# Kernel optimization log

Measured on AMD Instinct MI355X. Metric: run time of the kernel, lower is better.

## Reference

```python
import jax, jax.numpy as jnp
import numpy as np

NUM_HEADS = 8
EMBED_DIM = 128
TOTAL_TOKENS = 32768  # must be divisible by NUM_HEADS; per-head seq = 4096


def setup_inputs() -> dict:
    key = jax.random.key(0)
    ks = jax.random.split(key, 7)
    E, H, T = EMBED_DIM, NUM_HEADS, TOTAL_TOKENS
    return {
        "query": jax.random.normal(ks[0], (T, E), dtype=jnp.float32),
        "key": jax.random.normal(ks[1], (T, E), dtype=jnp.float32),    # unused by the module
        "value": jax.random.normal(ks[2], (T, E), dtype=jnp.float32),  # unused by the module
        "W_qkv": jax.random.normal(ks[3], (E, 3 * E), dtype=jnp.float32) * (1.0 / np.sqrt(E)),
        "b_qkv": jax.random.normal(ks[4], (3 * E,), dtype=jnp.float32) * 0.02,
        "u_bias": jax.random.normal(ks[5], (H, E), dtype=jnp.float32) * 0.02,
        "v_bias": jax.random.normal(ks[6], (H, E), dtype=jnp.float32) * 0.02,
    }


def reference(query, key, value, W_qkv, b_qkv, u_bias, v_bias):
    H, E = NUM_HEADS, EMBED_DIM
    # Fused QKV projection (torch Linear: x @ W; W stored [in, 3*out] here)
    qkv = query @ W_qkv + b_qkv                      # [T, 3E]
    q, k, v = jnp.split(qkv, 3, axis=-1)             # each [T, E]

    def heads(x):
        # view(-1, H, E).transpose(0, 1): token axis is split across heads
        return jnp.swapaxes(x.reshape(-1, H, E), 0, 1)  # [H, S, E], S = T // H

    q = heads(q) + u_bias[:, None, :]                # per-head additive bias on q
    k = heads(k) + v_bias[:, None, :]                # per-head additive bias on k
    v = heads(v)

    scale = 1.0 / jnp.sqrt(jnp.asarray(E, dtype=q.dtype))
    scores = jnp.einsum('hse,hte->hst', q, k) * scale  # [H, S, S]
    attn = jax.nn.softmax(scores, axis=-1)
    return jnp.einsum('hst,hte->hse', attn, v)         # [H, S, E]
```

## Files before the change

### kernel.cpp

```cpp
#include <hip/hip_runtime.h>
#include <hip/hip_bf16.h>
#include <stdint.h>

#define NHEADS 8
#define SEQ    4096
#define DIM    128
#define TOK    32768

typedef __attribute__((ext_vector_type(4)))  float  f32x4;
typedef __attribute__((ext_vector_type(16))) float  f32x16;
typedef __attribute__((ext_vector_type(8)))  short  bf16x8;
typedef __attribute__((ext_vector_type(8)))  unsigned short u16x8;
typedef __attribute__((ext_vector_type(4)))  unsigned int   u32x4;

__device__ __forceinline__ unsigned short f32_to_bf16(float f) {
  union { float f; unsigned int u; } cv; cv.f = f;
  unsigned int u = cv.u;
  u += 0x7FFFu + ((u >> 16) & 1u);
  return (unsigned short)(u >> 16);
}
__device__ __forceinline__ unsigned cvtpk(float lo, float hi) {
  unsigned r;
  asm("v_cvt_pk_bf16_f32 %0, %1, %2" : "=v"(r) : "v"(lo), "v"(hi));
  return r;
}
__device__ __forceinline__ void gload16(const void* g, void* l) {
  __builtin_amdgcn_global_load_lds(
      (const __attribute__((address_space(1))) unsigned int*)g,
      (__attribute__((address_space(3))) unsigned int*)l, 16, 0, 0);
}

__global__ __launch_bounds__(256) void wt_prep_kernel(
    const float* __restrict__ W, unsigned short* __restrict__ Wt) {
  const int tid = threadIdx.x;
  const int j  = blockIdx.x * 32 + (tid >> 3);
  const int k0 = (tid & 7) * 16;
  u16x8 a, b;
  #pragma unroll
  for (int x = 0; x < 8; ++x) a[x] = f32_to_bf16(W[(size_t)(k0 + x) * 384 + j]);
  #pragma unroll
  for (int x = 0; x < 8; ++x) b[x] = f32_to_bf16(W[(size_t)(k0 + 8 + x) * 384 + j]);
  *reinterpret_cast<u16x8*>(Wt + (size_t)j * 128 + k0)     = a;
  *reinterpret_cast<u16x8*>(Wt + (size_t)j * 128 + k0 + 8) = b;
}

__global__ __launch_bounds__(256, 2) void qkv_proj_kernel(
    const float* __restrict__ qin, const unsigned short* __restrict__ Wt,
    const float* __restrict__ bqkv, const float* __restrict__ ubias,
    const float* __restrict__ vbias,
    unsigned short* __restrict__ Qh, unsigned short* __restrict__ Kh,
    unsigned short* __restrict__ Vh) {
  __shared__ __align__(16) char Xl[16384];

  const int tid  = threadIdx.x;
  const int lane = tid & 63;
  const int w    = tid >> 6;
  const int wm   = w & 1;
  const int wn   = w >> 1;
  const int col  = lane & 31;
  const int hi   = lane >> 5;
  const int tok0 = blockIdx.x * 64;

  #pragma unroll
  for (int c = 0; c < 4; ++c) {
    int idx = tid + c * 256;
    int row = idx >> 4, c16 = idx & 15;
    const float* src = qin + (size_t)(tok0 + row) * DIM + c16 * 8;
    f32x4 lo  = *reinterpret_cast<const f32x4*>(src);
    f32x4 hi4 = *reinterpret_cast<const f32x4*>(src + 4);
    u32x4 pk;
    pk[0] = cvtpk(lo[0],  lo[1]);  pk[1] = cvtpk(lo[2],  lo[3]);
    pk[2] = cvtpk(hi4[0], hi4[1]); pk[3] = cvtpk(hi4[2], hi4[3]);
    *reinterpret_cast<u32x4*>(Xl + ((row * 256 + c16 * 16) ^ ((row & 7) << 4))) = pk;
  }
  __syncthreads();

  bf16x8 af[8];
  {
    int row = wm * 32 + col;
    #pragma unroll
    for (int kk = 0; kk < 8; ++kk)
      af[kk] = *reinterpret_cast<const bf16x8*>(
          Xl + ((row * 256 + kk * 32 + hi * 16) ^ ((row & 7) << 4)));
  }

  const int s0 = blockIdx.x * 8 + wm * 4;
  const float scale = 0.1275174309f;

  #pragma unroll
  for (int nt = 0; nt < 6; ++nt) {
    const int j0 = wn * 192 + nt * 32;

    const unsigned short* wp = Wt + (size_t)(j0 + col) * 128 + hi * 8;
    f32x16 acc = (f32x16)(0.0f);
    #pragma unroll
    for (int kk = 0; kk < 8; ++kk) {
      bf16x8 bf = *reinterpret_cast<const bf16x8*>(wp + kk * 16);
      acc = __builtin_amdgcn_mfma_f32_32x32x16_bf16(af[kk], bf, acc, 0, 0, 0);
    }

    const float bqv = bqkv[j0 + col];
    if (j0 < 128) {
      const int e = j0 + col;
      float ub[4];
      #pragma unroll
      for (int r = 0; r < 4; ++r) ub[r] = ubias[(r + 4 * hi) * DIM + e];
      #pragma unroll
      for (int i = 0; i < 16; ++i) {
        int h = (i & 3) + 4 * hi;
        Qh[((size_t)h * SEQ + s0 + (i >> 2)) * DIM + e] =
            f32_to_bf16((acc[i] + bqv + ub[i & 3]) * scale);
      }
    } else if (j0 < 256) {
      const int e = j0 - 128 + col;
      float vb[4];
      #pragma unroll
      for (int r = 0; r < 4; ++r) vb[r] = vbias[(r + 4 * hi) * DIM + e];
      #pragma unroll
      for (int i = 0; i < 16; ++i) {
        int h = (i & 3) + 4 * hi;
        Kh[((size_t)h * SEQ + s0 + (i >> 2)) * DIM + e] =
            f32_to_bf16(acc[i] + bqv + vb[i & 3]);
      }
    } else {
      const int e = j0 - 256 + col;
      #pragma unroll
      for (int i = 0; i < 16; ++i) {
        int h = (i & 3) + 4 * hi;
        Vh[((size_t)h * SEQ + s0 + (i >> 2)) * DIM + e] =
            f32_to_bf16(acc[i] + bqv);
      }
    }
  }
}

__global__ __launch_bounds__(256) void v_transpose_kernel(
    const unsigned short* __restrict__ Vh, unsigned short* __restrict__ Vt) {
  __shared__ unsigned short tile[64][66];
  const int h   = blockIdx.z;
  const int st  = blockIdx.y;
  const int et  = blockIdx.x;
  const int tid = threadIdx.x;

  #pragma unroll
  for (int c = 0; c < 2; ++c) {
    int idx = tid + c * 256;
    int sl  = idx >> 3;
    int e8  = idx & 7;
    u16x8 v = *reinterpret_cast<const u16x8*>(
        Vh + ((size_t)h * SEQ + st * 64 + sl) * DIM + et * 64 + e8 * 8);
    #pragma unroll
    for (int j = 0; j < 8; ++j) tile[sl][e8 * 8 + j] = v[j];
  }
  __syncthreads();
  #pragma unroll
  for (int c = 0; c < 2; ++c) {
    int idx = tid + c * 256;
    int el  = idx >> 3;
    int s8  = idx & 7;
    u16x8 v;
    #pragma unroll
    for (int j = 0; j < 8; ++j) v[j] = tile[s8 * 8 + j][el];
    *reinterpret_cast<u16x8*>(
        Vt + ((size_t)h * DIM + et * 64 + el) * SEQ + st * 64 + s8 * 8) = v;
  }
}

__global__ __launch_bounds__(768, 3) void attn_fwd_kernel(
    const unsigned short* __restrict__ Qh, const unsigned short* __restrict__ Kh,
    const unsigned short* __restrict__ Vt, float* __restrict__ Out) {
  __shared__ __align__(16) char smem[134656];
  float* lbuf = reinterpret_cast<float*>(smem + 131072);
  float* linv = reinterpret_cast<float*>(smem + 134144);

  const int tid  = threadIdx.x;
  const int lane = tid & 63;
  const int w    = tid >> 6;
  const int g    = w >> 2;
  const int wq   = w & 3;
  const int col  = lane & 31;
  const int hi   = lane >> 5;
  const int h    = blockIdx.x & 7;
  const int qb   = blockIdx.x >> 3;
  const int q0   = qb * 128 + wq * 32;

  const int tbase = g * 43;
  const int nt    = (g == 2) ? 42 : 43;

  char* Kg = smem + g * 16384;
  char* Vg = smem + 49152 + g * 20480;

  bf16x8 qf[8];
  const unsigned short* qp = Qh + ((size_t)h * SEQ + q0 + col) * DIM + hi * 8;
  #pragma unroll
  for (int kk = 0; kk < 8; ++kk)
    qf[kk] = *reinterpret_cast<const bf16x8*>(qp + kk * 16);

  f32x16 acc[4];
  #pragma unroll
  for (int n = 0; n < 4; ++n) acc[n] = (f32x16)(0.0f);
  float l_r = 0.0f;

  const int c3 = (col >> 1) & 3;
  const char* kpre[4];
  #pragma unroll
  for (int j = 0; j < 4; ++j)
    kpre[j] = Kg + col * 256 + ((hi ^ (col & 1)) << 4) + ((j ^ c3) << 5);
  const char* vb = Vg + col * 80 + hi * 16;

  int kofs[2];
  #pragma unroll
  for (int c2 = 0; c2 < 2; ++c2) {
    int c   = wq * 2 + c2;
    int row = c * 4 + (lane >> 4);
    kofs[c2] = row * 256 + ((((lane & 15) ^ (row & 7)) << 4));
  }
  int vofs[3];
  #pragma unroll
  for (int c2 = 0; c2 < 3; ++c2) {
    int c     = wq + 4 * c2;
    int laddr = c * 1024 + lane * 16;
    int row   = laddr / 80;
    int unit  = (laddr - row * 80) >> 4;
    vofs[c2]  = row * (SEQ * 2) + (unit < 4 ? unit * 16 : 0);
  }

  const char* KbaseB = reinterpret_cast<const char*>(Kh + (size_t)h * SEQ * DIM);
  const char* VbaseB = reinterpret_cast<const char*>(Vt + (size_t)h * DIM * SEQ);

  auto stage = [&](int tl, int buf) {
    const char* ks = KbaseB + (size_t)(tbase + tl) * 8192;
    #pragma unroll
    for (int c2 = 0; c2 < 2; ++c2)
      gload16(ks + kofs[c2], Kg + buf * 8192 + (wq * 2 + c2) * 1024);
    const char* vs = VbaseB + (size_t)(tbase + tl) * 64;
    #pragma unroll
    for (int c2 = 0; c2 < 3; ++c2) {
      int c = wq + 4 * c2;
      if (c < 10)
        gload16(vs + vofs[c2], Vg + buf * 10240 + c * 1024);
    }
  };

  auto compute = [&](int cur) {
    f32x16 sc = (f32x16)(0.0f);
    __builtin_amdgcn_s_setprio(1);
    #pragma unroll
    for (int kk = 0; kk < 8; ++kk) {
      bf16x8 kf = *reinterpret_cast<const bf16x8*>(
          kpre[kk & 3] + cur * 8192 + (kk >> 2) * 128);
      sc = __builtin_amdgcn_mfma_f32_32x32x16_bf16(kf, qf[kk], sc, 0, 0, 0);
    }
    __builtin_amdgcn_s_setprio(0);

    bf16x8 pa[2];
    #pragma unroll
    for (int s16 = 0; s16 < 2; ++s16) {
      float p8[8];
      #pragma unroll
      for (int i = 0; i < 8; ++i) {
        p8[i] = exp2f(sc[s16 * 8 + i]);
        l_r += p8[i];
      }
      unsigned A = cvtpk(p8[0], p8[1]);
      unsigned B = cvtpk(p8[4], p8[5]);
      asm("v_permlane32_swap_b32 %0, %1" : "+v"(A), "+v"(B));
      unsigned C = cvtpk(p8[2], p8[3]);
      unsigned D = cvtpk(p8[6], p8[7]);
      asm("v_permlane32_swap_b32 %0, %1" : "+v"(C), "+v"(D));
      u32x4 wd; wd[0] = A; wd[1] = C; wd[2] = B; wd[3] = D;
      pa[s16] = *reinterpret_cast<bf16x8*>(&wd);
    }

    bf16x8 vf0[2], vf1[2];
    #pragma unroll
    for (int ks = 0; ks < 2; ++ks) {
      vf0[ks] = *reinterpret_cast<const bf16x8*>(vb + cur * 10240 + ks * 32);
      vf1[ks] = *reinterpret_cast<const bf16x8*>(vb + cur * 10240 + 2560 + ks * 32);
    }
    __builtin_amdgcn_s_setprio(1);
    #pragma unroll
    for (int ks = 0; ks < 2; ++ks) {
      acc[0] = __builtin_amdgcn_mfma_f32_32x32x16_bf16(pa[ks], vf0[ks], acc[0], 0, 0, 0);
      acc[1] = __builtin_amdgcn_mfma_f32_32x32x16_bf16(pa[ks], vf1[ks], acc[1], 0, 0, 0);
    }
    __builtin_amdgcn_s_setprio(0);
    #pragma unroll
    for (int ks = 0; ks < 2; ++ks) {
      vf0[ks] = *reinterpret_cast<const bf16x8*>(vb + cur * 10240 + 5120 + ks * 32);
      vf1[ks] = *reinterpret_cast<const bf16x8*>(vb + cur * 10240 + 7680 + ks * 32);
    }
    __builtin_amdgcn_s_setprio(1);
    #pragma unroll
    for (int ks = 0; ks < 2; ++ks) {
      acc[2] = __builtin_amdgcn_mfma_f32_32x32x16_bf16(pa[ks], vf0[ks], acc[2], 0, 0, 0);
      acc[3] = __builtin_amdgcn_mfma_f32_32x32x16_bf16(pa[ks], vf1[ks], acc[3], 0, 0, 0);
    }
    __builtin_amdgcn_s_setprio(0);
  };

  stage(0, 0);
  __syncthreads();

  stage(1, 1);
  compute(0);
  __syncthreads();

  for (int t2 = 0; t2 < 21; ++t2) {
    const int t = 2 * t2 + 1;
    if (t + 1 < nt) stage(t + 1, 0);
    compute(1);
    __syncthreads();
    if (t + 2 < nt) stage(t + 2, 1);
    if (t + 1 < nt) compute(0);
    __syncthreads();
  }

  lbuf[w * 64 + lane] = l_r;
  if (g > 0) {
    char* mb = smem + ((g - 1) * 4 + wq) * 16384;
    #pragma unroll
    for (int n = 0; n < 4; ++n)
      #pragma unroll
      for (int i = 0; i < 4; ++i) {
        f32x4 v;
        v[0] = acc[n][4 * i + 0]; v[1] = acc[n][4 * i + 1];
        v[2] = acc[n][4 * i + 2]; v[3] = acc[n][4 * i + 3];
        *reinterpret_cast<f32x4*>(mb + (n * 4 + i) * 1024 + lane * 16) = v;
      }
  }
  __syncthreads();
  if (g == 0) {
    #pragma unroll
    for (int s = 0; s < 2; ++s) {
      const char* mb = smem + (s * 4 + wq) * 16384;
      #pragma unroll
      for (int n = 0; n < 4; ++n)
        #pragma unroll
        for (int i = 0; i < 4; ++i) {
          f32x4 v = *reinterpret_cast<const f32x4*>(mb + (n * 4 + i) * 1024 + lane * 16);
          acc[n][4 * i + 0] += v[0]; acc[n][4 * i + 1] += v[1];
          acc[n][4 * i + 2] += v[2]; acc[n][4 * i + 3] += v[3];
        }
    }
    float ltot = 0.0f;
    #pragma unroll
    for (int gg = 0; gg < 3; ++gg)
      ltot += lbuf[(gg * 4 + wq) * 64 + col] + lbuf[(gg * 4 + wq) * 64 + col + 32];
    linv[wq * 32 + col] = 1.0f / ltot;
    asm volatile("s_waitcnt lgkmcnt(0)" ::: "memory");

    float* op = Out + ((size_t)h * SEQ + q0) * DIM + col;
    #pragma unroll
    for (int g2 = 0; g2 < 4; ++g2) {
      f32x4 iv = *reinterpret_cast<f32x4*>(&linv[wq * 32 + 8 * g2 + 4 * hi]);
      #pragma unroll
      for (int n = 0; n < 4; ++n)
        #pragma unroll
        for (int i = 0; i < 4; ++i)
          op[(size_t)(8 * g2 + 4 * hi + i) * DIM + n * 32] =
              acc[n][4 * g2 + i] * iv[i];
    }
  }
}

extern "C" void kernel_launch(void* const* d_in, const int* in_sizes, int n_in,
                              void* d_out, int out_size, void* d_ws, size_t ws_size,
                              hipStream_t stream) {
  (void)in_sizes; (void)n_in; (void)out_size; (void)ws_size;
  const float* query = (const float*)d_in[0];
  const float* W_qkv = (const float*)d_in[3];
  const float* b_qkv = (const float*)d_in[4];
  const float* u_bias = (const float*)d_in[5];
  const float* v_bias = (const float*)d_in[6];
  float* out = (float*)d_out;

  const size_t per = (size_t)NHEADS * SEQ * DIM;
  unsigned short* Qh = (unsigned short*)d_ws;
  unsigned short* Kh = Qh + per;
  unsigned short* Vh = Kh + per;
  unsigned short* Vt = Vh + per;
  unsigned short* Wt = Vt;

  wt_prep_kernel<<<dim3(12), dim3(256), 0, stream>>>(W_qkv, Wt);
  qkv_proj_kernel<<<dim3(TOK / 64), dim3(256), 0, stream>>>(
      query, Wt, b_qkv, u_bias, v_bias, Qh, Kh, Vh);
  v_transpose_kernel<<<dim3(2, 64, 8), dim3(256), 0, stream>>>(Vh, Vt);
  attn_fwd_kernel<<<dim3(NHEADS * 32), dim3(768), 0, stream>>>(Qh, Kh, Vt, out);
}
```

Baseline: 118.9 us.

## Fuse V transpose into QKV projection and stage Q/V writes through LDS

The QKV projection now writes its Q and V results into shared-memory staging buffers, then stores Q with coalesced 16-byte writes and writes V already transposed into the Vt layout. This removes the separate V transpose kernel launch and its extra global read and write of V. It also moves Wt into its own workspace slot, since Vt is now written while Wt is still being read. The cost is 32 KB more shared memory per block, which may reduce occupancy of the projection kernel, and an extra barrier.

```diff
diff --git a/kernel.cpp b/kernel.cpp
--- a/kernel.cpp
+++ b/kernel.cpp
@@ -49,8 +49,10 @@
     const float* __restrict__ bqkv, const float* __restrict__ ubias,
     const float* __restrict__ vbias,
     unsigned short* __restrict__ Qh, unsigned short* __restrict__ Kh,
-    unsigned short* __restrict__ Vh) {
+    unsigned short* __restrict__ Vt) {
   __shared__ __align__(16) char Xl[16384];
+  __shared__ __align__(16) unsigned short Qb[8192];
+  __shared__ __align__(16) unsigned short Vb[8192];
 
   const int tid  = threadIdx.x;
   const int lane = tid & 63;
@@ -60,6 +62,7 @@
   const int col  = lane & 31;
   const int hi   = lane >> 5;
   const int tok0 = blockIdx.x * 64;
+  const int s0b  = blockIdx.x * 8;
 
   #pragma unroll
   for (int c = 0; c < 4; ++c) {
@@ -84,7 +87,7 @@
           Xl + ((row * 256 + kk * 32 + hi * 16) ^ ((row & 7) << 4)));
   }
 
-  const int s0 = blockIdx.x * 8 + wm * 4;
+  const int s0 = s0b + wm * 4;
   const float scale = 0.1275174309f;
 
   #pragma unroll
@@ -108,8 +111,8 @@
       #pragma unroll
       for (int i = 0; i < 16; ++i) {
         int h = (i & 3) + 4 * hi;
-        Qh[((size_t)h * SEQ + s0 + (i >> 2)) * DIM + e] =
-            f32_to_bf16((acc[i] + bqv + ub[i & 3]) * scale);
+        int s = wm * 4 + (i >> 2);
+        Qb[h * 1024 + s * 128 + e] = f32_to_bf16((acc[i] + bqv + ub[i & 3]) * scale);
       }
     } else if (j0 < 256) {
       const int e = j0 - 128 + col;
@@ -127,42 +130,29 @@
       #pragma unroll
       for (int i = 0; i < 16; ++i) {
         int h = (i & 3) + 4 * hi;
-        Vh[((size_t)h * SEQ + s0 + (i >> 2)) * DIM + e] =
-            f32_to_bf16(acc[i] + bqv);
-      }
-    }
-  }
-}
-
-__global__ __launch_bounds__(256) void v_transpose_kernel(
-    const unsigned short* __restrict__ Vh, unsigned short* __restrict__ Vt) {
-  __shared__ unsigned short tile[64][66];
-  const int h   = blockIdx.z;
-  const int st  = blockIdx.y;
-  const int et  = blockIdx.x;
-  const int tid = threadIdx.x;
-
-  #pragma unroll
-  for (int c = 0; c < 2; ++c) {
-    int idx = tid + c * 256;
-    int sl  = idx >> 3;
-    int e8  = idx & 7;
-    u16x8 v = *reinterpret_cast<const u16x8*>(
-        Vh + ((size_t)h * SEQ + st * 64 + sl) * DIM + et * 64 + e8 * 8);
-    #pragma unroll
-    for (int j = 0; j < 8; ++j) tile[sl][e8 * 8 + j] = v[j];
-  }
-  __syncthreads();
-  #pragma unroll
-  for (int c = 0; c < 2; ++c) {
-    int idx = tid + c * 256;
-    int el  = idx >> 3;
-    int s8  = idx & 7;
+        int s = wm * 4 + (i >> 2);
+        Vb[h * 1024 + s * 128 + e] = f32_to_bf16(acc[i] + bqv);
+      }
+    }
+  }
+
+  __syncthreads();
+
+  #pragma unroll
+  for (int p = 0; p < 4; ++p) {
+    int cid = tid + p * 256;
+    int h = cid >> 7, s = (cid >> 4) & 7, ec = cid & 15;
+    u16x8 v = *reinterpret_cast<const u16x8*>(&Qb[h * 1024 + s * 128 + ec * 8]);
+    *reinterpret_cast<u16x8*>(Qh + ((size_t)h * SEQ + s0b + s) * DIM + ec * 8) = v;
+  }
+  #pragma unroll
+  for (int p = 0; p < 4; ++p) {
+    int cid = tid + p * 256;
+    int h = cid >> 7, e = cid & 127;
     u16x8 v;
     #pragma unroll
-    for (int j = 0; j < 8; ++j) v[j] = tile[s8 * 8 + j][el];
-    *reinterpret_cast<u16x8*>(
-        Vt + ((size_t)h * DIM + et * 64 + el) * SEQ + st * 64 + s8 * 8) = v;
+    for (int sl = 0; sl < 8; ++sl) v[sl] = Vb[h * 1024 + sl * 128 + e];
+    *reinterpret_cast<u16x8*>(Vt + ((size_t)h * DIM + e) * SEQ + s0b) = v;
   }
 }
 
@@ -378,13 +368,11 @@
   const size_t per = (size_t)NHEADS * SEQ * DIM;
   unsigned short* Qh = (unsigned short*)d_ws;
   unsigned short* Kh = Qh + per;
-  unsigned short* Vh = Kh + per;
-  unsigned short* Vt = Vh + per;
-  unsigned short* Wt = Vt;
+  unsigned short* Wt = Kh + per;
+  unsigned short* Vt = Wt + per;
 
   wt_prep_kernel<<<dim3(12), dim3(256), 0, stream>>>(W_qkv, Wt);
   qkv_proj_kernel<<<dim3(TOK / 64), dim3(256), 0, stream>>>(
-      query, Wt, b_qkv, u_bias, v_bias, Qh, Kh, Vh);
-  v_transpose_kernel<<<dim3(2, 64, 8), dim3(256), 0, stream>>>(Vh, Vt);
+      query, Wt, b_qkv, u_bias, v_bias, Qh, Kh, Vt);
   attn_fwd_kernel<<<dim3(NHEADS * 32), dim3(768), 0, stream>>>(Qh, Kh, Vt, out);
 }
```

Measured after the change: 118.0 us, median of 2. No clear change (-0.8%).
